# Performance work log

Hardware: AMD Instinct MI355X
Metric: run time of the kernel (lower is better)

## Reference

```python
import jax, jax.numpy as jnp
import numpy as np

A_DIM = 18
HID = 512
LSTM_IN = HID + A_DIM + 1  # 531


def setup_inputs() -> dict:
    key = jax.random.key(0)
    ks = jax.random.split(key, 26)
    T, B = 80, 64
    inp = {}
    inp["o"] = jax.random.randint(ks[0], (T, B, 1, 84, 84), 0, 255, dtype=jnp.int32)
    inp["a"] = jax.random.randint(ks[1], (T, B), 0, A_DIM, dtype=jnp.int32)
    inp["r"] = jax.random.normal(ks[2], (T, B), dtype=jnp.float32)
    inp["done"] = jax.random.randint(ks[3], (T, B), 0, 2, dtype=jnp.int32)
    inp["h0"] = jnp.zeros((B, HID), dtype=jnp.float32)
    inp["c0"] = jnp.zeros((B, HID), dtype=jnp.float32)

    def gw(k, shape, s=0.05):
        return (jax.random.normal(k, shape, dtype=jnp.float32) * s)

    # CNN trunk params (torch Conv2d OIHW layout)
    inp["conv1_w"] = gw(ks[4], (32, 1, 8, 8))
    inp["conv1_b"] = jnp.zeros((32,), jnp.float32)
    inp["conv2_w"] = gw(ks[5], (64, 32, 4, 4))
    inp["conv2_b"] = jnp.zeros((64,), jnp.float32)
    inp["conv3_w"] = gw(ks[6], (64, 64, 3, 3))
    inp["conv3_b"] = jnp.zeros((64,), jnp.float32)
    inp["fc_w"] = gw(ks[7], (HID, 64 * 7 * 7))
    inp["fc_b"] = jnp.zeros((HID,), jnp.float32)
    # LSTM params (torch gate order: i, f, g, o)
    inp["W_ih"] = gw(ks[8], (4 * HID, LSTM_IN))
    inp["W_hh"] = gw(ks[9], (4 * HID, HID))
    inp["b_ih"] = jnp.zeros((4 * HID,), jnp.float32)
    inp["b_hh"] = jnp.zeros((4 * HID,), jnp.float32)
    # Dueling heads
    inp["adv_w1"] = gw(ks[10], (HID, HID))
    inp["adv_b1"] = jnp.zeros((HID,), jnp.float32)
    inp["adv_w2"] = gw(ks[11], (A_DIM, HID))
    inp["adv_b2"] = jnp.zeros((A_DIM,), jnp.float32)
    inp["val_w1"] = gw(ks[12], (HID, HID))
    inp["val_b1"] = jnp.zeros((HID,), jnp.float32)
    inp["val_w2"] = gw(ks[13], (1, HID))
    inp["val_b2"] = jnp.zeros((1,), jnp.float32)
    return inp


def _conv(x, w, b, stride):
    y = jax.lax.conv_general_dilated(
        x, w, (stride, stride), 'VALID',
        dimension_numbers=('NCHW', 'OIHW', 'NCHW'))
    return y + b[None, :, None, None]


def reference(o, a, r, done, h0, c0,
              conv1_w, conv1_b, conv2_w, conv2_b, conv3_w, conv3_b,
              fc_w, fc_b, W_ih, W_hh, b_ih, b_hh,
              adv_w1, adv_b1, adv_w2, adv_b2,
              val_w1, val_b1, val_w2, val_b2):
    T, B = o.shape[0], o.shape[1]
    x = o.reshape(T * B, 1, 84, 84).astype(jnp.float32) / 255.0
    x = jax.nn.relu(_conv(x, conv1_w, conv1_b, 4))   # [TB,32,20,20]
    x = jax.nn.relu(_conv(x, conv2_w, conv2_b, 2))   # [TB,64,9,9]
    x = jax.nn.relu(_conv(x, conv3_w, conv3_b, 1))   # [TB,64,7,7]
    x = x.reshape(T * B, 64 * 7 * 7)
    hidden = jax.nn.relu(x @ fc_w.T + fc_b).reshape(T, B, HID)

    a_one_hot = jax.nn.one_hot(a, A_DIM, dtype=jnp.float32)      # [T,B,A]
    lstm_in = jnp.concatenate([hidden, r[..., None], a_one_hot], axis=-1)  # [T,B,531]
    keep = (1.0 - done.astype(jnp.float32))[..., None]           # [T,B,1]
    bias = b_ih + b_hh

    def step(carry, inp_t):
        h, c = carry
        x_t, m = inp_t
        h = h * m
        c = c * m
        g = x_t @ W_ih.T + h @ W_hh.T + bias   # [B, 4H]
        i, f, gg, oo = jnp.split(g, 4, axis=-1)
        c = jax.nn.sigmoid(f) * c + jax.nn.sigmoid(i) * jnp.tanh(gg)
        h = jax.nn.sigmoid(oo) * jnp.tanh(c)
        return (h, c), h

    (hT, cT), hs = jax.lax.scan(step, (h0, c0), (lstm_in, keep))
    z = hs.reshape(T * B, HID)

    adv = jax.nn.relu(z @ adv_w1.T + adv_b1) @ adv_w2.T + adv_b2  # [TB,A]
    val = jax.nn.relu(z @ val_w1.T + val_b1) @ val_w2.T + val_b2  # [TB,1]
    q = val + (adv - adv.mean(axis=1, keepdims=True))
    return q.reshape(T, B, A_DIM), hT, cT
```

## Files before the change

### kernel.cpp

```cpp
#include <hip/hip_runtime.h>
#include <hip/hip_bf16.h>
#include <stdint.h>

typedef __bf16 bf16;
typedef __bf16 bfrag __attribute__((ext_vector_type(8)));
typedef short s16x8 __attribute__((ext_vector_type(8)));
typedef float f32x4 __attribute__((ext_vector_type(4)));
typedef float f32x16 __attribute__((ext_vector_type(16)));
typedef uint32_t u32x4 __attribute__((ext_vector_type(4)));

#define DEV __device__ __forceinline__

DEV bfrag ldg16(const bf16* p){ return *(const bfrag*)p; }

struct U64x2 { uint64_t a, b; };
DEV bfrag ld2x8(const bf16* p){
  U64x2 t; t.a = *(const uint64_t*)p; t.b = *(const uint64_t*)(p+4);
  return __builtin_bit_cast(bfrag, t);
}

DEV f32x4  mfma16(bfrag a, bfrag b, f32x4  c){ return __builtin_amdgcn_mfma_f32_16x16x32_bf16(a,b,c,0,0,0); }
DEV f32x16 mfma32(bfrag a, bfrag b, f32x16 c){ return __builtin_amdgcn_mfma_f32_32x32x16_bf16(a,b,c,0,0,0); }

DEV f32x16 zero16(){
  f32x16 v;
  for(int i=0;i<16;++i) v[i]=0.f;
  return v;
}
DEV f32x4 zero4(){
  f32x4 v;
  for(int i=0;i<4;++i) v[i]=0.f;
  return v;
}

DEV float sigm(float x){ return 1.0f/(1.0f+__expf(-x)); }
DEV float ftanh(float x){ float e = __expf(2.f*x); return 1.f - 2.f/(e+1.f); }

DEV u32x4 ldcg4(const uint32_t* p){
  u32x4 r;
  asm volatile("global_load_dwordx4 %0, %1, off sc0 sc1" : "=v"(r) : "v"(p));
  return r;
}

DEV uint32_t pk2f(float a, float b){
  bf16 x = (bf16)a, y = (bf16)b;
  return (uint32_t)__builtin_bit_cast(uint16_t,x) | ((uint32_t)__builtin_bit_cast(uint16_t,y)<<16);
}

__global__ __launch_bounds__(256) void k_prep(
    const float* __restrict__ c1w, const float* __restrict__ c2w,
    const float* __restrict__ c3w, const float* __restrict__ fcw,
    const float* __restrict__ Wih, const float* __restrict__ WhhF,
    const float* __restrict__ bih, const float* __restrict__ bhh,
    const float* __restrict__ aw1, const float* __restrict__ aw2,
    const float* __restrict__ vw1, const float* __restrict__ vw2,
    const float* __restrict__ h0,
    bf16* w1b, bf16* w2r, bf16* w3r, bf16* fcwr, bf16* Wx, bf16* Whh,
    float* biasL, float* Wr, float* Wa, bf16* headw1, float* headb1,
    bf16* w2cat, uint32_t* hcurT)
{
  long i = (long)blockIdx.x*256 + threadIdx.x;
  if (i < 2048){ int co=(int)(i>>6), k=(int)(i&63);
    w1b[i] = (bf16)(c1w[co*64+k]*(1.f/255.f)); return; } i -= 2048;
  if (i < 32768){ int o=(int)(i>>9), k=(int)(i&511);
    int ky=k>>7, kx=(k>>5)&3, ci=k&31;
    w2r[i] = (bf16)c2w[((o*32+ci)*4+ky)*4+kx]; return; } i -= 32768;
  if (i < 36864){ int o=(int)(i/576), k=(int)(i%576);
    int ky=k/192, rem=k-ky*192, kx=rem>>6, ci=rem&63;
    w3r[i] = (bf16)c3w[((o*64+ci)*3+ky)*3+kx]; return; } i -= 36864;
  if (i < 1638400){ int o=(int)(i/3200), k=(int)(i%3200);
    float v = 0.f;
    if (k < 3136){ int y=k/448, rem=k-y*448, x=rem>>6, ci=rem&63;
      v = fcw[o*3136 + ci*49 + y*7 + x]; }
    fcwr[i] = (bf16)v; return; } i -= 1638400;
  if (i < 1048576){ int n=(int)(i>>9), k=(int)(i&511);
    Wx[i] = (bf16)Wih[n*531+k]; return; } i -= 1048576;
  if (i < 1048576){ int n=(int)(i>>9), k=(int)(i&511);
    Whh[i] = (bf16)WhhF[n*512+k]; return; } i -= 1048576;
  if (i < 2048){ biasL[i] = bih[i]+bhh[i]; return; } i -= 2048;
  if (i < 2048){ Wr[i] = Wih[i*531+512]; return; } i -= 2048;
  if (i < 36864){ int j=(int)(i>>11), n=(int)(i&2047);
    Wa[i] = Wih[n*531+513+j]; return; } i -= 36864;
  if (i < 524288){ headw1[i] = (bf16)(i<262144 ? aw1[i] : vw1[i-262144]); return; } i -= 524288;
  if (i < 1024){ headb1[i] = 0.f; return; } i -= 1024;
  if (i < 32768){ int n=(int)(i>>10), k=(int)(i&1023);
    float v = 0.f;
    if (n<18 && k<512) v = aw2[n*512+k];
    else if (n==18 && k>=512) v = vw2[k-512];
    w2cat[i] = (bf16)v; return; } i -= 32768;
  if (i < 32768){
    if (i < 16384){
      int row = (int)(i>>8), wd = (int)(i&255);
      uint32_t pk = pk2f(h0[row*512 + wd*2], h0[row*512 + wd*2 + 1]);
      hcurT[i] = pk & ~0x00010001u;
    } else {
      hcurT[i] = 0x00010000u;
    }
    return;
  }
}

__global__ __launch_bounds__(256) void k_prep2(
    const float* __restrict__ ab1, const float* __restrict__ vb1, float* headb1)
{
  int i = blockIdx.x*256 + threadIdx.x;
  headb1[i] = (i<512) ? ab1[i] : vb1[i-512];
}

__global__ __launch_bounds__(512,1) void k_conv12(
    const int* __restrict__ o, const bf16* __restrict__ w1b,
    const float* __restrict__ c1b, const bf16* __restrict__ w2r,
    const float* __restrict__ c2b, bf16* __restrict__ act2)
{
  __shared__ bf16 simg[4][7056];
  __shared__ bf16 lact[4][12800];
  const int tid = threadIdx.x;
  const long imgbase = (long)blockIdx.x*4;
  const int4* src = (const int4*)o;
  for (int u = tid; u < 7056; u += 512){
    int4 v = src[imgbase*1764 + u];
    int il = u/1764, p4 = u - il*1764;
    uint32_t lo = (uint32_t)__builtin_bit_cast(uint16_t,(bf16)(float)v.x)
                | ((uint32_t)__builtin_bit_cast(uint16_t,(bf16)(float)v.y)<<16);
    uint32_t hi = (uint32_t)__builtin_bit_cast(uint16_t,(bf16)(float)v.z)
                | ((uint32_t)__builtin_bit_cast(uint16_t,(bf16)(float)v.w)<<16);
    *(uint64_t*)&simg[il][p4*4] = (uint64_t)lo | ((uint64_t)hi<<32);
  }
  __syncthreads();
  const int w = tid>>6, l = tid&63;
  const int img = w>>1, h = w&1;
  const bf16* sp = &simg[img][0];
  char* lw = (char*)&lact[img][0];
  {
    bfrag bw[4];
    #pragma unroll
    for (int ks=0;ks<4;++ks) bw[ks] = ldg16(w1b + (l&31)*64 + ks*16 + 8*(l>>5));
    const float bias = c1b[l&31];
    for (int mt=h; mt<13; mt+=2){
      f32x16 acc = zero16();
      int m0 = mt*32 + (l&31);
      int p  = m0>399 ? 399 : m0;
      int oy = p/20, ox = p - oy*20;
      #pragma unroll
      for (int ks=0;ks<4;++ks){
        int ky = 2*ks + (l>>5);
        bfrag a = ld2x8(sp + (oy*4+ky)*84 + ox*4);
        acc = mfma32(a, bw[ks], acc);
      }
      #pragma unroll
      for (int r2=0;r2<16;++r2){
        int row = (r2&3) + 8*(r2>>2) + 4*(l>>5);
        int m = mt*32 + row;
        if (m < 400){
          float v = acc[r2] + bias; v = v>0.f ? v : 0.f;
          *(bf16*)(lw + m*64 + (((l&31)*2) ^ ((m&3)<<4))) = (bf16)v;
        }
      }
    }
  }
  __syncthreads();
  {
    f32x16 acc2[3];
    #pragma unroll
    for (int a2=0;a2<3;++a2) acc2[a2]=zero16();
    int pb[3];
    #pragma unroll
    for (int mt=0;mt<3;++mt){
      int m = mt*32 + (l&31); int p = m>80 ? 80 : m;
      int oy = p/9, ox = p - oy*9;
      pb[mt] = (oy*2)*20 + ox*2;
    }
    #pragma unroll 4
    for (int ks=0; ks<32; ++ks){
      int k  = ks*16 + 8*(l>>5);
      int ky = k>>7, kx = (k>>5)&3, ci = k&31;
      bfrag b0 = ldg16(w2r + (32*h + (l&31))*512 + k);
      #pragma unroll
      for (int mt=0; mt<3; ++mt){
        int p2 = pb[mt] + ky*20 + kx;
        bfrag a = *(const bfrag*)(lw + p2*64 + ((ci*2) ^ ((p2&3)<<4)));
        acc2[mt] = mfma32(a, b0, acc2[mt]);
      }
    }
    const float bias2 = c2b[32*h + (l&31)];
    #pragma unroll
    for (int mt=0; mt<3; ++mt){
      #pragma unroll
      for (int r2=0;r2<16;++r2){
        int row = (r2&3) + 8*(r2>>2) + 4*(l>>5);
        int m = mt*32 + row;
        if (m < 81){
          float v = acc2[mt][r2] + bias2; v = v>0.f ? v : 0.f;
          act2[(imgbase+img)*5184 + m*64 + 32*h + (l&31)] = (bf16)v;
        }
      }
    }
  }
}

__global__ __launch_bounds__(256,2) void k_conv3(
    const bf16* __restrict__ act2, const bf16* __restrict__ w3r,
    const float* __restrict__ c3b, bf16* __restrict__ act3)
{
  const int tid=threadIdx.x, w=tid>>6, l=tid&63;
  const long img = (long)blockIdx.x*4 + w;
  const bf16* A = act2 + img*5184;
  f32x16 acc[2][2];
  #pragma unroll
  for(int a2=0;a2<2;++a2){ acc[a2][0]=zero16(); acc[a2][1]=zero16(); }
  #pragma unroll 4
  for (int ks=0; ks<36; ++ks){
    int k  = ks*16 + 8*(l>>5);
    int ky = k/192, rem = k - ky*192, kx = rem>>6, ci = rem&63;
    bfrag b0 = ldg16(w3r + (l&31)*576 + k);
    bfrag b1 = ldg16(w3r + (32+(l&31))*576 + k);
    #pragma unroll
    for (int mt=0; mt<2; ++mt){
      int m = mt*32 + (l&31); int p = m>48 ? 48 : m;
      int oy = p/7, ox = p - oy*7;
      bfrag a = ldg16(A + ((oy+ky)*9 + (ox+kx))*64 + ci);
      acc[mt][0] = mfma32(a, b0, acc[mt][0]);
      acc[mt][1] = mfma32(a, b1, acc[mt][1]);
    }
  }
  const float bias0 = c3b[l&31], bias1 = c3b[32+(l&31)];
  #pragma unroll
  for (int mt=0; mt<2; ++mt){
    #pragma unroll
    for (int r2=0;r2<16;++r2){
      int row = (r2&3) + 8*(r2>>2) + 4*(l>>5);
      int m = mt*32 + row;
      if (m < 50){
        float v0 = 0.f, v1 = 0.f;
        if (m < 49){
          v0 = acc[mt][0][r2] + bias0; v0 = v0>0.f ? v0 : 0.f;
          v1 = acc[mt][1][r2] + bias1; v1 = v1>0.f ? v1 : 0.f;
        }
        act3[img*3200 + m*64 + (l&31)]      = (bf16)v0;
        act3[img*3200 + m*64 + 32 + (l&31)] = (bf16)v1;
      }
    }
  }
}

template<bool RELU, bool OUTBF16>
__global__ __launch_bounds__(256,4) void k_gemm(
    const bf16* __restrict__ A, long lda,
    const bf16* __restrict__ W, long ldb,
    const float* __restrict__ bias,
    float* __restrict__ outF, bf16* __restrict__ outB, long ldo, int K,
    const float* __restrict__ fixR, const int* __restrict__ fixA,
    const float* __restrict__ fixWr, const float* __restrict__ fixWa)
{
  __shared__ bf16 sA[8192];
  char* sb = (char*)sA;
  const int tid=threadIdx.x, w=tid>>6, l=tid&63;
  const int m0 = blockIdx.x*64, n0 = blockIdx.y*128;
  f32x16 acc[2]; acc[0]=zero16(); acc[1]=zero16();
  const int mt = w&1;
  const int rowa = mt*32 + (l&31);
  for (int kc=0; kc<K; kc+=128){
    __syncthreads();
    for (int u = tid; u < 1024; u += 256){
      int row = u>>4, seg = u&15;
      s16x8 v = *(const s16x8*)(A + (long)(m0+row)*lda + kc + seg*8);
      *(s16x8*)(sb + row*256 + ((seg*16) ^ ((row&15)<<4))) = v;
    }
    __syncthreads();
    #pragma unroll
    for (int ks=0; ks<8; ++ks){
      bfrag a = *(const bfrag*)(sb + rowa*256 + ((ks*32 + (l>>5)*16) ^ ((rowa&15)<<4)));
      #pragma unroll
      for (int j=0;j<2;++j){
        int nt = (w>>1)*2 + j;
        bfrag b = ldg16(W + (long)(n0 + nt*32 + (l&31))*ldb + kc + ks*16 + 8*(l>>5));
        acc[j] = mfma32(a, b, acc[j]);
      }
    }
  }
  #pragma unroll
  for (int j=0;j<2;++j){
    int nt = (w>>1)*2 + j;
    int gc = n0 + nt*32 + (l&31);
    float bv = bias ? bias[gc] : 0.f;
    float wrv = fixR ? fixWr[gc] : 0.f;
    #pragma unroll
    for (int r2=0;r2<16;++r2){
      int row = (r2&3) + 8*(r2>>2) + 4*(l>>5);
      long gr = m0 + mt*32 + row;
      float v = acc[j][r2] + bv;
      if (fixR) v += fixR[gr]*wrv + fixWa[(long)fixA[gr]*2048 + gc];
      if (RELU) v = v>0.f ? v : 0.f;
      if (OUTBF16) outB[gr*ldo + gc] = (bf16)v;
      else         outF[gr*ldo + gc] = v;
    }
  }
}

__global__ __launch_bounds__(256,1) void k_lstm(
    const float* __restrict__ G, const int* __restrict__ done,
    const float* __restrict__ c0, const bf16* __restrict__ Whh,
    uint32_t* __restrict__ hcurT, bf16* __restrict__ hseq,
    float* __restrict__ outH, float* __restrict__ outC)
{
  __shared__ bf16 swt[65536];
  __shared__ bf16 sh2[8192];
  __shared__ float sg[4][16][33];
  __shared__ float sc[16][33];
  __shared__ char  sdone[80][16];
  const int tid=threadIdx.x, w=tid>>6, l=tid&63;
  const int blk=blockIdx.x;
  const int grp=(blk&7)>>1, jj=((blk&1)<<3)|(blk>>3);
  const int bb = grp*16, uu = jj*32;

  for (int p=tid; p<512; p+=256){ int m=p>>5, u=p&31; sc[m][u] = c0[(bb+m)*512 + uu + u]; }
  for (int p=tid; p<1280; p+=256){ int t=p>>4, m=p&15; sdone[t][m] = (char)done[t*64 + bb + m]; }

  char* swb = (char*)swt;
  for (int u = tid; u < 8192; u += 256){
    int wg = u>>11, ks2 = (u>>6)&31, ll = u&63;
    int row = uu + (ll&15) + ((ks2&1)<<4);
    int k   = (ks2>>1)*32 + 8*(ll>>4);
    bfrag v = ldg16(Whh + ((long)wg*512 + row)*512 + k);
    *(bfrag*)(swb + ((u*16) ^ ((ks2&7)<<4))) = v;
  }

  char* shb = (char*)sh2;
  const char* wbase = swb + w*32768;
  const int loff = l*16;
  const int srow  = tid>>4;
  const int sci   = tid&15;

  __syncthreads();

  for (int t=0; t<80; ++t){
    float gv0[4], gv1[4];
    {
      const float* Gt = G + ((long)t*64 + bb)*2048 + w*512 + uu;
      #pragma unroll
      for (int r2=0;r2<4;++r2){
        int m2 = (l>>4)*4 + r2;
        gv0[r2] = Gt[(long)m2*2048 + (l&15)];
        gv1[r2] = Gt[(long)m2*2048 + 16 + (l&15)];
      }
    }
    __builtin_amdgcn_sched_barrier(0);
    {
      const uint32_t* hb = hcurT + (size_t)(t&1)*16384 + (size_t)(bb+srow)*256 + sci*16;
      u32x4 hv[4];
      const uint32_t expPat = ((uint32_t)(t&1)) | (((uint32_t)((t>>1)&1))<<16);
      for (;;){
        #pragma unroll
        for (int j2=0;j2<4;++j2) hv[j2] = ldcg4(hb + j2*4);
        asm volatile("s_waitcnt vmcnt(0)" ::: "memory");
        bool ok = true;
        #pragma unroll
        for (int j2=0;j2<4;++j2){
          ok &= ((hv[j2][0]&0x00010001u)==expPat) & ((hv[j2][1]&0x00010001u)==expPat)
              & ((hv[j2][2]&0x00010001u)==expPat) & ((hv[j2][3]&0x00010001u)==expPat);
        }
        if (__all(ok)) break;
        __builtin_amdgcn_s_sleep(1);
      }
      if (sdone[t][srow]){
        #pragma unroll
        for (int j2=0;j2<4;++j2){ u32x4 z = {0,0,0,0}; hv[j2] = z; }
      } else {
        #pragma unroll
        for (int j2=0;j2<4;++j2){
          hv[j2][0] &= ~0x00010001u; hv[j2][1] &= ~0x00010001u;
          hv[j2][2] &= ~0x00010001u; hv[j2][3] &= ~0x00010001u;
        }
      }
      #pragma unroll
      for (int j=0;j<4;++j){
        *(u32x4*)(shb + sci*1024 + ((((srow + 16*j)*16)) ^ ((sci&7)<<4))) = hv[j];
      }
    }
    __syncthreads();
    f32x4 a0e = zero4(), a0o = zero4(), a1e = zero4(), a1o = zero4();
    #pragma unroll
    for (int ks=0; ks<16; ++ks){
      bfrag a  = *(const bfrag*)(shb + ks*1024 + (loff ^ ((ks&7)<<4)));
      bfrag b0 = *(const bfrag*)(wbase + (2*ks)*1024   + (loff ^ (((2*ks)&7)<<4)));
      bfrag b1 = *(const bfrag*)(wbase + (2*ks+1)*1024 + (loff ^ (((2*ks+1)&7)<<4)));
      if (ks & 1){ a0o = mfma16(a, b0, a0o); a1o = mfma16(a, b1, a1o); }
      else       { a0e = mfma16(a, b0, a0e); a1e = mfma16(a, b1, a1e); }
    }
    #pragma unroll
    for (int r2=0;r2<4;++r2){
      int m = (l>>4)*4 + r2;
      sg[w][m][(l&15)]    = a0e[r2] + a0o[r2] + gv0[r2];
      sg[w][m][16+(l&15)] = a1e[r2] + a1o[r2] + gv1[r2];
    }
    __syncthreads();
    {
      int p0 = tid*2; int m = p0>>5, u = p0&31;
      int dn = sdone[t][m];
      float c_0 = dn ? 0.f : sc[m][u];
      float c_1 = dn ? 0.f : sc[m][u+1];
      float i0=sg[0][m][u],   f0=sg[1][m][u],   g0=sg[2][m][u],   o0=sg[3][m][u];
      float i1=sg[0][m][u+1], f1=sg[1][m][u+1], g1=sg[2][m][u+1], o1=sg[3][m][u+1];
      float cn0 = sigm(f0)*c_0 + sigm(i0)*ftanh(g0);
      float cn1 = sigm(f1)*c_1 + sigm(i1)*ftanh(g1);
      float h_0 = sigm(o0)*ftanh(cn0);
      float h_1 = sigm(o1)*ftanh(cn1);
      sc[m][u] = cn0; sc[m][u+1] = cn1;
      uint32_t pk = pk2f(h_0, h_1);
      int p1 = (t+1)&3;
      uint32_t pat = ((uint32_t)(p1&1)) | (((uint32_t)(p1>>1))<<16);
      uint32_t pkT = (pk & ~0x00010001u) | pat;
      __hip_atomic_store(
          hcurT + (size_t)((t+1)&1)*16384 + (size_t)(bb+m)*256 + ((uu+u)>>1),
          pkT, __ATOMIC_RELAXED, __HIP_MEMORY_SCOPE_AGENT);
      *(uint32_t*)(hseq + ((long)t*64 + bb + m)*512 + uu + u) = pk;
      if (t == 79){
        outH[(bb+m)*512 + uu + u]   = h_0;  outH[(bb+m)*512 + uu + u+1] = h_1;
        outC[(bb+m)*512 + uu + u]   = cn0;  outC[(bb+m)*512 + uu + u+1] = cn1;
      }
    }
  }
}

__global__ __launch_bounds__(256) void k_qhead(
    const bf16* __restrict__ zav, const bf16* __restrict__ w2cat,
    const float* __restrict__ ab2, const float* __restrict__ vb2,
    float* __restrict__ q)
{
  __shared__ float sq[4][16][33];
  const int tid=threadIdx.x, w=tid>>6, l=tid&63;
  const int s0 = blockIdx.x*64 + w*16;
  f32x4 acc0 = zero4(), acc1 = zero4();
  const int row = l&15;
  #pragma unroll 4
  for (int ks=0; ks<32; ++ks){
    int k = ks*32 + 8*(l>>4);
    bfrag a  = ldg16(zav + (long)(s0+row)*1024 + k);
    bfrag b0 = ldg16(w2cat + (l&15)*1024 + k);
    bfrag b1 = ldg16(w2cat + (16+(l&15))*1024 + k);
    acc0 = mfma16(a, b0, acc0);
    acc1 = mfma16(a, b1, acc1);
  }
  #pragma unroll
  for (int r2=0;r2<4;++r2){
    int m = (l>>4)*4 + r2;
    sq[w][m][l&15]      = acc0[r2];
    sq[w][m][16+(l&15)] = acc1[r2];
  }
  __syncthreads();
  if (l < 16){
    int s = s0 + l;
    float av[18]; float sum = 0.f;
    #pragma unroll
    for (int j=0;j<18;++j){ av[j] = sq[w][l][j] + ab2[j]; sum += av[j]; }
    float val = sq[w][l][18] + vb2[0];
    float mean = sum * (1.f/18.f);
    #pragma unroll
    for (int j=0;j<18;++j) q[(long)s*18 + j] = val + av[j] - mean;
  }
}

extern "C" void kernel_launch(void* const* d_in, const int* in_sizes, int n_in,
                              void* d_out, int out_size, void* d_ws, size_t ws_size,
                              hipStream_t stream)
{
  (void)in_sizes; (void)n_in; (void)out_size;
  const int*   o_in = (const int*)  d_in[0];
  const int*   a_in = (const int*)  d_in[1];
  const float* r_in = (const float*)d_in[2];
  const int*   done = (const int*)  d_in[3];
  const float* h0   = (const float*)d_in[4];
  const float* c0   = (const float*)d_in[5];
  const float* c1w  = (const float*)d_in[6],  *c1b=(const float*)d_in[7];
  const float* c2w  = (const float*)d_in[8],  *c2b=(const float*)d_in[9];
  const float* c3w  = (const float*)d_in[10], *c3b=(const float*)d_in[11];
  const float* fcw  = (const float*)d_in[12], *fcb=(const float*)d_in[13];
  const float* Wih  = (const float*)d_in[14], *WhhF=(const float*)d_in[15];
  const float* bih  = (const float*)d_in[16], *bhh=(const float*)d_in[17];
  const float* aw1  = (const float*)d_in[18], *ab1=(const float*)d_in[19];
  const float* aw2  = (const float*)d_in[20], *ab2=(const float*)d_in[21];
  const float* vw1  = (const float*)d_in[22], *vb1=(const float*)d_in[23];
  const float* vw2  = (const float*)d_in[24], *vb2=(const float*)d_in[25];

  char* ws = (char*)d_ws;
  size_t off = 0;
  auto alloc = [&](size_t b){ size_t p = off; off = (off + b + 255) & ~(size_t)255; return p; };
  bf16*  act2   = (bf16*) (ws + alloc(53084160));
  bf16*  act3   = (bf16*) (ws + alloc(32768000));
  bf16*  hidden = (bf16*) (ws + alloc(5242880));
  uint32_t* hcurT = (uint32_t*)(ws + alloc(131072));
  bf16*  w1b    = (bf16*) (ws + alloc(4096));
  bf16*  w2r    = (bf16*) (ws + alloc(65536));
  bf16*  w3r    = (bf16*) (ws + alloc(73728));
  bf16*  fcwr   = (bf16*) (ws + alloc(3276800));
  bf16*  Wx     = (bf16*) (ws + alloc(2097152));
  bf16*  Whh    = (bf16*) (ws + alloc(2097152));
  float* biasL  = (float*)(ws + alloc(8192));
  float* Wr     = (float*)(ws + alloc(8192));
  float* Wa     = (float*)(ws + alloc(147456));
  bf16*  headw1 = (bf16*) (ws + alloc(1048576));
  float* headb1 = (float*)(ws + alloc(4096));
  bf16*  w2cat  = (bf16*) (ws + alloc(65536));
  if (off > ws_size) return;

  float* G    = (float*)act2;
  bf16*  hseq = hidden;
  bf16*  zav  = act3;

  float* qout = (float*)d_out;
  float* outH = qout + 92160;
  float* outC = qout + 124928;

  k_prep<<<17340, 256, 0, stream>>>(c1w, c2w, c3w, fcw, Wih, WhhF, bih, bhh,
      aw1, aw2, vw1, vw2, h0, w1b, w2r, w3r, fcwr, Wx, Whh,
      biasL, Wr, Wa, headw1, headb1, w2cat, hcurT);
  k_prep2<<<4, 256, 0, stream>>>(ab1, vb1, headb1);

  k_conv12<<<1280, 512, 0, stream>>>(o_in, w1b, c1b, w2r, c2b, act2);
  k_conv3<<<1280, 256, 0, stream>>>(act2, w3r, c3b, act3);
  k_gemm<true,true><<<dim3(80,4), 256, 0, stream>>>(
      act3, 3200, fcwr, 3200, fcb, nullptr, hidden, 512, 3200,
      nullptr, nullptr, nullptr, nullptr);
  k_gemm<false,false><<<dim3(80,16), 256, 0, stream>>>(
      hidden, 512, Wx, 512, biasL, G, nullptr, 2048, 512,
      r_in, a_in, Wr, Wa);

  k_lstm<<<64, 256, 0, stream>>>(G, done, c0, Whh, hcurT, hseq, outH, outC);

  k_gemm<true,true><<<dim3(80,8), 256, 0, stream>>>(
      hseq, 512, headw1, 512, headb1, nullptr, zav, 1024, 512,
      nullptr, nullptr, nullptr, nullptr);
  k_qhead<<<80, 256, 0, stream>>>(zav, w2cat, ab2, vb2, qout);
}
```

Baseline: 653.0 us.

## Read conv1 input directly from global, shrink conv12 blocks, fold prep2 into prep

The conv12 kernel no longer stages the int32 image in shared memory. Each lane loads its 8x8 patch rows straight from global memory and converts them to bf16 in registers. Blocks now handle 2 images with 256 threads instead of 4 with 512, launch bounds allow 2 blocks per CU, and the conv1 activation layout in LDS moves from an XOR swizzle to a padded 72-byte row stride. The separate head-bias prep kernel is merged into k_prep to remove one launch. The trade-off is that overlapping patches are now read redundantly from global or cache, in exchange for less LDS, more occupancy and no staging barrier.

```diff
diff --git a/kernel.cpp b/kernel.cpp
--- a/kernel.cpp
+++ b/kernel.cpp
@@ -54,7 +54,8 @@
     const float* __restrict__ bih, const float* __restrict__ bhh,
     const float* __restrict__ aw1, const float* __restrict__ aw2,
     const float* __restrict__ vw1, const float* __restrict__ vw2,
-    const float* __restrict__ h0,
+    const float* __restrict__ h0, const float* __restrict__ ab1,
+    const float* __restrict__ vb1,
     bf16* w1b, bf16* w2r, bf16* w3r, bf16* fcwr, bf16* Wx, bf16* Whh,
     float* biasL, float* Wr, float* Wa, bf16* headw1, float* headb1,
     bf16* w2cat, uint32_t* hcurT)
@@ -82,7 +83,7 @@
   if (i < 36864){ int j=(int)(i>>11), n=(int)(i&2047);
     Wa[i] = Wih[n*531+513+j]; return; } i -= 36864;
   if (i < 524288){ headw1[i] = (bf16)(i<262144 ? aw1[i] : vw1[i-262144]); return; } i -= 524288;
-  if (i < 1024){ headb1[i] = 0.f; return; } i -= 1024;
+  if (i < 1024){ headb1[i] = (i<512) ? ab1[i] : vb1[i-512]; return; } i -= 1024;
   if (i < 32768){ int n=(int)(i>>10), k=(int)(i&1023);
     float v = 0.f;
     if (n<18 && k<512) v = aw2[n*512+k];
@@ -100,36 +101,17 @@
   }
 }
 
-__global__ __launch_bounds__(256) void k_prep2(
-    const float* __restrict__ ab1, const float* __restrict__ vb1, float* headb1)
-{
-  int i = blockIdx.x*256 + threadIdx.x;
-  headb1[i] = (i<512) ? ab1[i] : vb1[i-512];
-}
-
-__global__ __launch_bounds__(512,1) void k_conv12(
+__global__ __launch_bounds__(256,2) void k_conv12(
     const int* __restrict__ o, const bf16* __restrict__ w1b,
     const float* __restrict__ c1b, const bf16* __restrict__ w2r,
     const float* __restrict__ c2b, bf16* __restrict__ act2)
 {
-  __shared__ bf16 simg[4][7056];
-  __shared__ bf16 lact[4][12800];
+  __shared__ bf16 lact[2][14400];
   const int tid = threadIdx.x;
-  const long imgbase = (long)blockIdx.x*4;
-  const int4* src = (const int4*)o;
-  for (int u = tid; u < 7056; u += 512){
-    int4 v = src[imgbase*1764 + u];
-    int il = u/1764, p4 = u - il*1764;
-    uint32_t lo = (uint32_t)__builtin_bit_cast(uint16_t,(bf16)(float)v.x)
-                | ((uint32_t)__builtin_bit_cast(uint16_t,(bf16)(float)v.y)<<16);
-    uint32_t hi = (uint32_t)__builtin_bit_cast(uint16_t,(bf16)(float)v.z)
-                | ((uint32_t)__builtin_bit_cast(uint16_t,(bf16)(float)v.w)<<16);
-    *(uint64_t*)&simg[il][p4*4] = (uint64_t)lo | ((uint64_t)hi<<32);
-  }
-  __syncthreads();
   const int w = tid>>6, l = tid&63;
   const int img = w>>1, h = w&1;
-  const bf16* sp = &simg[img][0];
+  const long gimg = (long)blockIdx.x*2 + img;
+  const int* ip = o + gimg*7056;
   char* lw = (char*)&lact[img][0];
   {
     bfrag bw[4];
@@ -144,7 +126,14 @@
       #pragma unroll
       for (int ks=0;ks<4;++ks){
         int ky = 2*ks + (l>>5);
-        bfrag a = ld2x8(sp + (oy*4+ky)*84 + ox*4);
+        const int* q = ip + (oy*4+ky)*84 + ox*4;
+        int4 i0 = *(const int4*)q;
+        int4 i1 = *(const int4*)(q+4);
+        bfrag a;
+        a[0]=(bf16)(float)i0.x; a[1]=(bf16)(float)i0.y;
+        a[2]=(bf16)(float)i0.z; a[3]=(bf16)(float)i0.w;
+        a[4]=(bf16)(float)i1.x; a[5]=(bf16)(float)i1.y;
+        a[6]=(bf16)(float)i1.z; a[7]=(bf16)(float)i1.w;
         acc = mfma32(a, bw[ks], acc);
       }
       #pragma unroll
@@ -153,7 +142,7 @@
         int m = mt*32 + row;
         if (m < 400){
           float v = acc[r2] + bias; v = v>0.f ? v : 0.f;
-          *(bf16*)(lw + m*64 + (((l&31)*2) ^ ((m&3)<<4))) = (bf16)v;
+          *(bf16*)(lw + m*72 + (l&31)*2) = (bf16)v;
         }
       }
     }
@@ -178,7 +167,7 @@
       #pragma unroll
       for (int mt=0; mt<3; ++mt){
         int p2 = pb[mt] + ky*20 + kx;
-        bfrag a = *(const bfrag*)(lw + p2*64 + ((ci*2) ^ ((p2&3)<<4)));
+        bfrag a = ld2x8((const bf16*)(lw + p2*72) + ci);
         acc2[mt] = mfma32(a, b0, acc2[mt]);
       }
     }
@@ -191,7 +180,7 @@
         int m = mt*32 + row;
         if (m < 81){
           float v = acc2[mt][r2] + bias2; v = v>0.f ? v : 0.f;
-          act2[(imgbase+img)*5184 + m*64 + 32*h + (l&31)] = (bf16)v;
+          act2[gimg*5184 + m*64 + 32*h + (l&31)] = (bf16)v;
         }
       }
     }
@@ -512,11 +501,10 @@
   float* outC = qout + 124928;
 
   k_prep<<<17340, 256, 0, stream>>>(c1w, c2w, c3w, fcw, Wih, WhhF, bih, bhh,
-      aw1, aw2, vw1, vw2, h0, w1b, w2r, w3r, fcwr, Wx, Whh,
+      aw1, aw2, vw1, vw2, h0, ab1, vb1, w1b, w2r, w3r, fcwr, Wx, Whh,
       biasL, Wr, Wa, headw1, headb1, w2cat, hcurT);
-  k_prep2<<<4, 256, 0, stream>>>(ab1, vb1, headb1);
-
-  k_conv12<<<1280, 512, 0, stream>>>(o_in, w1b, c1b, w2r, c2b, act2);
+
+  k_conv12<<<2560, 256, 0, stream>>>(o_in, w1b, c1b, w2r, c2b, act2);
   k_conv3<<<1280, 256, 0, stream>>>(act2, w3r, c3b, act3);
   k_gemm<true,true><<<dim3(80,4), 256, 0, stream>>>(
       act3, 3200, fcwr, 3200, fcb, nullptr, hidden, 512, 3200,
```

Result: faster. 621.0 us (-4.9%).
